# Kernel tuning notes

Measured on AMD Instinct MI355X. Metric: run time of the kernel, lower is better.

## Reference

```python
import jax, jax.numpy as jnp
import numpy as np

LMBD = 0.1      # cfg['MODEL']['LAMBDA'][0]
MU = 0.1        # ISTA/FISTA step size (cfg['MODEL']['MU'])
N_STEPS = 4     # cfg['MODEL']['NUM_LAYERS']
FISTA = True    # cfg['MODEL']['ISFISTA']


def _conv(x, W, s, p):
    # torch F.conv2d, NCHW / OIHW
    return jax.lax.conv_general_dilated(x, W, (s, s), [(p, p), (p, p)],
        dimension_numbers=('NCHW', 'OIHW', 'NCHW'))


def _conv_t(z, W, s, p):
    # torch F.conv_transpose2d(z, W, stride=s, padding=p): output (H-1)*s + k - 2p
    k = W.shape[-1]
    Wt = jnp.transpose(jnp.flip(W, (-2, -1)), (1, 0, 2, 3))
    pad = k - 1 - p
    return jax.lax.conv_general_dilated(z, Wt, (1, 1), [(pad, pad), (pad, pad)],
        lhs_dilation=(s, s), dimension_numbers=('NCHW', 'OIHW', 'NCHW'))


def _wnorm(W):
    # per-atom unit-norm dictionary (w_norm=True)
    return W / (jnp.sqrt(jnp.sum(W * W, axis=(1, 2, 3), keepdims=True)) + 1e-12)


def _dict_block(x, W, s, p):
    # unrolled FISTA sparse coding: min_z 0.5||x - W^T*z||^2 + lmbd||z||_1, z>=0
    thr = MU * LMBD
    shrink = lambda u: jax.nn.relu(u - thr)  # non-negative soft threshold
    z0 = shrink(MU * _conv(x, W, s, p))

    def body(carry, _):
        z, z_old, t = carry
        if FISTA:
            t_new = (1.0 + jnp.sqrt(1.0 + 4.0 * t * t)) * 0.5
            y = z + ((t - 1.0) / t_new) * (z - z_old)
        else:
            t_new, y = t, z
        r = x - _conv_t(y, W, s, p)                 # residual in image space
        z_new = shrink(y + MU * _conv(r, W, s, p))  # gradient step + shrinkage
        return (z_new, z, t_new), None

    (z, _, _), _ = jax.lax.scan(body, (z0, z0, jnp.float32(1.0)), None, length=N_STEPS - 1)
    return z


def _bn(x, eps=1e-5):
    # BatchNorm2d at init (gamma=1, beta=0), training-mode batch stats, biased var
    m = jnp.mean(x, axis=(0, 2, 3), keepdims=True)
    v = jnp.var(x, axis=(0, 2, 3), keepdims=True)
    return (x - m) * jax.lax.rsqrt(v + eps)


def _lrelu(x):
    return jnp.where(x >= 0, x, 0.2 * x)


def setup_inputs() -> dict:
    key = jax.random.key(0)
    ks = jax.random.split(key, 7)
    nc, ndf, nz = 3, 64, 128

    def kaiming(k, shape):
        fan_in = shape[1] * shape[2] * shape[3]
        bound = float(np.sqrt(6.0 / fan_in))
        return jax.random.uniform(k, shape, jnp.float32, -bound, bound)

    return {
        'x':  jax.random.normal(ks[0], (64, nc, 96, 96), jnp.float32),
        'W1': kaiming(ks[1], (ndf, nc, 4, 4)),
        'W2': kaiming(ks[2], (ndf * 2, ndf, 4, 4)),
        'W3': kaiming(ks[3], (ndf * 4, ndf * 2, 4, 4)),
        'W4': kaiming(ks[4], (ndf * 8, ndf * 4, 4, 4)),
        'W5': kaiming(ks[5], (ndf * 16, ndf * 8, 4, 4)),
        'W6': kaiming(ks[6], (nz, ndf * 16, 3, 3)),
    }


def reference(x, W1, W2, W3, W4, W5, W6):
    Ws = [_wnorm(w) for w in (W1, W2, W3, W4, W5, W6)]
    # encoder: 96 -> 48 -> 24 -> 12 -> 6 -> 3 -> 1
    o = _lrelu(_dict_block(x, Ws[0], 2, 1))
    for i in range(1, 5):
        o = _lrelu(_bn(_dict_block(o, Ws[i], 2, 1)))
    z = _dict_block(o, Ws[5], 1, 0).reshape(x.shape[0], -1)
    z = z / jnp.maximum(jnp.linalg.norm(z, axis=1, keepdims=True), 1e-12)  # F.normalize
    # decoder (DictConv2d.inverse chain, uses the normalized dictionaries)
    h = z.reshape(z.shape[0], -1, 1, 1)
    h = jax.nn.relu(_bn(_conv_t(h, Ws[5], 1, 0)))
    for i in (4, 3, 2, 1):
        h = jax.nn.relu(_bn(_conv_t(h, Ws[i], 2, 1)))
    x_hat = jnp.tanh(_conv_t(h, Ws[0], 2, 1))
    return z, x_hat
```

## Files before the change

kernel.cpp:

```cpp
#include <hip/hip_runtime.h>
#include <math.h>

#define BLK 256
static constexpr float MU_F  = 0.1f;
static constexpr float THR_F = 0.01f;

typedef __attribute__((ext_vector_type(8))) short bf16x8;
typedef __attribute__((ext_vector_type(4))) float f32x4;

__device__ inline unsigned short f2bf(float f) {
    unsigned u = __float_as_uint(f);
    unsigned r = (u + 0x7fffu + ((u >> 16) & 1u)) >> 16;
    return (unsigned short)r;
}
__device__ inline float bf2f(unsigned short h) {
    return __uint_as_float(((unsigned)h) << 16);
}

__device__ inline float blk_reduce(float v) {
    __shared__ float sh[BLK];
    int tid = threadIdx.x;
    sh[tid] = v;
    __syncthreads();
    #pragma unroll
    for (int s = BLK / 2; s > 0; s >>= 1) {
        if (tid < s) sh[tid] += sh[tid + s];
        __syncthreads();
    }
    float r = sh[0];
    __syncthreads();
    return r;
}

__global__ __launch_bounds__(BLK) void wnorm_pack(
    const float* __restrict__ W, float* __restrict__ Wkc,
    float* __restrict__ Wnout, int Mout, int asz)
{
    int o = blockIdx.x;
    const float* w = W + (size_t)o * asz;
    float s = 0.f;
    for (int i = threadIdx.x; i < asz; i += BLK) { float v = w[i]; s = fmaf(v, v, s); }
    float tot = blk_reduce(s);
    float inv = 1.0f / (sqrtf(tot) + 1e-12f);
    for (int i = threadIdx.x; i < asz; i += BLK) {
        float v = w[i] * inv;
        Wkc[(size_t)i * Mout + o] = v;
        if (Wnout) Wnout[(size_t)o * asz + i] = v;
    }
}

__global__ __launch_bounds__(BLK) void wnorm_pack_bf16(
    const float* __restrict__ W, short* __restrict__ Cpk, short* __restrict__ Tpk,
    int Cout, int Cin)
{
    int o = blockIdx.x;
    int asz = Cin * 16;
    const float* w = W + (size_t)o * asz;
    float s = 0.f;
    for (int i = threadIdx.x; i < asz; i += BLK) { float v = w[i]; s = fmaf(v, v, s); }
    float tot = blk_reduce(s);
    float inv = 1.0f / (sqrtf(tot) + 1e-12f);
    size_t cTot = (size_t)Cout * asz;
    size_t parStride = (size_t)Cout * 4 * Cin;
    size_t tTot = 4 * parStride;
    for (int i = threadIdx.x; i < asz; i += BLK) {
        float v = w[i] * inv;
        unsigned short hb = f2bf(v);
        unsigned short lb = f2bf(v - bf2f(hb));
        size_t cidx = ((size_t)(i >> 3)) * (Cout * 8) + o * 8 + (i & 7);
        Cpk[cidx] = (short)hb;
        Cpk[cTot + cidx] = (short)lb;
        int c = i >> 4, tap = i & 15, kh = tap >> 2, kw = tap & 3;
        int par = (1 - (kh & 1)) * 2 + (1 - (kw & 1));
        int tt = ((kh >> 1) << 1) | (kw >> 1);
        int q = o * 4 + tt;
        size_t tidx = (size_t)par * parStride + ((size_t)(q >> 3)) * (Cin * 8) + c * 8 + (q & 7);
        Tpk[tidx] = (short)hb;
        Tpk[tTot + tidx] = (short)lb;
    }
}

__device__ inline void xcd_remap(int& bx, int& by, int& bz) {
    int nx = gridDim.x, ny = gridDim.y;
    int nwg = nx * ny * gridDim.z;
    int orig = blockIdx.x + nx * (blockIdx.y + ny * blockIdx.z);
    int q8 = nwg >> 3, r8 = nwg & 7, xcd = orig & 7, sidx = orig >> 3;
    int w = (xcd < r8 ? xcd * (q8 + 1) : r8 * (q8 + 1) + (xcd - r8) * q8) + sidx;
    bx = w % nx; int t = w / nx; by = t % ny; bz = t / ny;
}

__global__ __launch_bounds__(BLK) void conv_gemm_bf16(
    const short* __restrict__ Wpk, const float* __restrict__ x,
    const float* __restrict__ yin, float* __restrict__ out,
    int M, int Cx, int Hx, int Wx, int Hout, int Wout,
    int kchunk, int emode)
{
    __shared__ __align__(16) short Wh[4][64][8];
    __shared__ __align__(16) short Wo_[4][64][8];
    __shared__ __align__(16) short Xh[4][64][8];
    __shared__ __align__(16) short Xo[4][64][8];
    int bx, by, bz; xcd_remap(bx, by, bz);
    int tid = threadIdx.x, lane = tid & 63, wid = tid >> 6;
    int HW = Hout * Wout, HWx = Hx * Wx;
    int pbase = bx * 64, m0 = by * 64, kb = bz * kchunk;
    size_t loOff = (size_t)Cx * 16 * M;

    int spl = tid & 63, skb = tid >> 6;
    int sp = pbase + spl;
    int sn = sp / HW; int srr = sp - sn * HW;
    int sho = srr / Wout, swo = srr - sho * Wout;
    const float* xs = x + (size_t)sn * Cx * HWx;
    int h0 = sho * 2 - 1, w0 = swo * 2 - 1;

    f32x4 acc[4] = {};
    for (int k0 = kb; k0 < kb + kchunk; k0 += 32) {
        size_t so = ((size_t)((k0 >> 3) + skb)) * (M * 8) + (size_t)m0 * 8 + spl * 8;
        *(float4*)(&Wh[skb][spl][0])  = *(const float4*)(Wpk + so);
        *(float4*)(&Wo_[skb][spl][0]) = *(const float4*)(Wpk + loOff + so);
        {
            int kbase = k0 + skb * 8;
            int ci = kbase >> 4;
            int t16 = kbase & 15;
            const float* xc = xs + (size_t)ci * HWx;
            union { short s[8]; float4 f; } uh, ul;
            #pragma unroll
            for (int jj = 0; jj < 8; ++jj) {
                int tap = t16 + jj;
                int kh = tap >> 2, kw = tap & 3;
                int h = h0 + kh, w = w0 + kw;
                float g = ((unsigned)h < (unsigned)Hx && (unsigned)w < (unsigned)Wx)
                        ? xc[h * Wx + w] : 0.f;
                unsigned short hb = f2bf(g);
                uh.s[jj] = (short)hb;
                ul.s[jj] = (short)f2bf(g - bf2f(hb));
            }
            *(float4*)(&Xh[skb][spl][0]) = uh.f;
            *(float4*)(&Xo[skb][spl][0]) = ul.f;
        }
        __syncthreads();
        bf16x8 ah = *(const bf16x8*)(&Wh[lane >> 4][wid * 16 + (lane & 15)][0]);
        bf16x8 al = *(const bf16x8*)(&Wo_[lane >> 4][wid * 16 + (lane & 15)][0]);
        #pragma unroll
        for (int nf = 0; nf < 4; ++nf) {
            bf16x8 bh = *(const bf16x8*)(&Xh[lane >> 4][nf * 16 + (lane & 15)][0]);
            bf16x8 bl = *(const bf16x8*)(&Xo[lane >> 4][nf * 16 + (lane & 15)][0]);
            acc[nf] = __builtin_amdgcn_mfma_f32_16x16x32_bf16(al, bh, acc[nf], 0, 0, 0);
            acc[nf] = __builtin_amdgcn_mfma_f32_16x16x32_bf16(ah, bl, acc[nf], 0, 0, 0);
            acc[nf] = __builtin_amdgcn_mfma_f32_16x16x32_bf16(ah, bh, acc[nf], 0, 0, 0);
        }
        __syncthreads();
    }
    int colp = lane & 15, rquad = lane >> 4;
    #pragma unroll
    for (int nf = 0; nf < 4; ++nf) {
        int p = pbase + nf * 16 + colp;
        int n = p / HW; int rr = p - n * HW;
        int ho = rr / Wout, wo = rr - ho * Wout;
        #pragma unroll
        for (int r = 0; r < 4; ++r) {
            int m = m0 + wid * 16 + rquad * 4 + r;
            size_t idx = (((size_t)n * M + m) * Hout + ho) * Wout + wo;
            float v = acc[nf][r];
            if (emode == 0)      out[idx] = fmaxf(MU_F * v - THR_F, 0.f);
            else if (emode == 1) out[idx] = fmaxf(yin[idx] + MU_F * v - THR_F, 0.f);
            else                 atomicAdd(&out[idx], v);
        }
    }
}

__global__ __launch_bounds__(BLK) void convt_gemm_bf16(
    const short* __restrict__ Wpk, const float* __restrict__ z,
    const float* __restrict__ aux, float* __restrict__ out,
    int M, int Cz, int Hz, int Wz, int Ho, int Wo, int emode, int SK)
{
    __shared__ __align__(16) short Wh[4][64][8];
    __shared__ __align__(16) short Wo_[4][64][8];
    __shared__ __align__(16) short Xh[4][64][8];
    __shared__ __align__(16) short Xo[4][64][8];
    int bx, by, bz; xcd_remap(bx, by, bz);
    int tid = threadIdx.x, lane = tid & 63, wid = tid >> 6;
    int par = bz / SK, chunk = bz - par * SK;
    int hbit = par >> 1, wbit = par & 1;
    int czs = Cz / SK;
    int qb = chunk * czs * 4;
    size_t parS = (size_t)Cz * 4 * M;
    const short* Wp = Wpk + (size_t)par * parS;
    size_t loOff = 4 * parS;
    int Hc = Ho >> 1, Wc = Wo >> 1, HWc = Hc * Wc;
    int pbase = bx * 64, m0 = by * 64;

    int spl = tid & 63, skb = tid >> 6;
    int sp = pbase + spl;
    int sn = sp / HWc; int srr = sp - sn * HWc;
    int shc = srr / Wc, swc = srr - shc * Wc;
    const float* zs = z + (size_t)sn * Cz * Hz * Wz;

    f32x4 acc[4] = {};
    for (int q0 = qb; q0 < qb + czs * 4; q0 += 32) {
        size_t so = ((size_t)((q0 >> 3) + skb)) * (M * 8) + (size_t)m0 * 8 + spl * 8;
        *(float4*)(&Wh[skb][spl][0])  = *(const float4*)(Wp + so);
        *(float4*)(&Wo_[skb][spl][0]) = *(const float4*)(Wp + loOff + so);
        {
            int qq = q0 + skb * 8;
            union { short s[8]; float4 f; } uh, ul;
            #pragma unroll
            for (int jj = 0; jj < 8; ++jj) {
                int q = qq + jj;
                int cz = q >> 2, tt = q & 3, ti = tt >> 1, tj = tt & 1;
                int hn = shc + hbit - ti, wn = swc + wbit - tj;
                float g = ((unsigned)hn < (unsigned)Hz && (unsigned)wn < (unsigned)Wz)
                        ? zs[((size_t)cz * Hz + hn) * Wz + wn] : 0.f;
                unsigned short hb = f2bf(g);
                uh.s[jj] = (short)hb;
                ul.s[jj] = (short)f2bf(g - bf2f(hb));
            }
            *(float4*)(&Xh[skb][spl][0]) = uh.f;
            *(float4*)(&Xo[skb][spl][0]) = ul.f;
        }
        __syncthreads();
        bf16x8 ah = *(const bf16x8*)(&Wh[lane >> 4][wid * 16 + (lane & 15)][0]);
        bf16x8 al = *(const bf16x8*)(&Wo_[lane >> 4][wid * 16 + (lane & 15)][0]);
        #pragma unroll
        for (int nf = 0; nf < 4; ++nf) {
            bf16x8 bh = *(const bf16x8*)(&Xh[lane >> 4][nf * 16 + (lane & 15)][0]);
            bf16x8 bl = *(const bf16x8*)(&Xo[lane >> 4][nf * 16 + (lane & 15)][0]);
            acc[nf] = __builtin_amdgcn_mfma_f32_16x16x32_bf16(al, bh, acc[nf], 0, 0, 0);
            acc[nf] = __builtin_amdgcn_mfma_f32_16x16x32_bf16(ah, bl, acc[nf], 0, 0, 0);
            acc[nf] = __builtin_amdgcn_mfma_f32_16x16x32_bf16(ah, bh, acc[nf], 0, 0, 0);
        }
        __syncthreads();
    }
    int colp = lane & 15, rquad = lane >> 4;
    #pragma unroll
    for (int nf = 0; nf < 4; ++nf) {
        int p = pbase + nf * 16 + colp;
        int n = p / HWc; int rr = p - n * HWc;
        int hc = rr / Wc, wc = rr - hc * Wc;
        int ho = 2 * hc + hbit, wo = 2 * wc + wbit;
        #pragma unroll
        for (int r = 0; r < 4; ++r) {
            int m = m0 + wid * 16 + rquad * 4 + r;
            size_t idx = (((size_t)n * M + m) * Ho + ho) * Wo + wo;
            float v = acc[nf][r];
            if (emode == 0)      out[idx] = aux[idx] - v;
            else if (emode == 1) out[idx] = v;
            else                 atomicAdd(&out[idx], v);
        }
    }
}

template <int KK, int Kk, int S, int P>
__global__ __launch_bounds__(BLK) void conv_gemm(
    const float* __restrict__ Wp, const float* __restrict__ x,
    const float* __restrict__ yin, float* __restrict__ out,
    int M, int Ktot, int Cx, int Hx, int Wx, int Hout, int Wout,
    int kchunk, int emode)
{
    __shared__ float Wt[16][64];
    __shared__ float Xt[16][64];
    int tid = threadIdx.x, tx = tid & 15, ty = tid >> 4;
    int HW = Hout * Wout, HWx = Hx * Wx;
    int pbase = blockIdx.x * 64 + tx * 4;
    int n_[4], ho_[4], wo_[4];
    const float* xb_[4];
    #pragma unroll
    for (int j = 0; j < 4; ++j) {
        int p = pbase + j; int n = p / HW; int r = p - n * HW;
        int ho = r / Wout; int wo = r - ho * Wout;
        n_[j] = n; ho_[j] = ho; wo_[j] = wo;
        xb_[j] = x + (size_t)n * Cx * HWx;
    }
    int m0 = blockIdx.y * 64;
    int kb = blockIdx.z * kchunk, ke = kb + kchunk;
    if (ke > Ktot) ke = Ktot;
    float acc[4][4] = {};
    for (int k0 = kb; k0 < ke; k0 += 16) {
        int kr = k0 + ty;
        *(float4*)&Wt[ty][tx * 4] = *(const float4*)&Wp[(size_t)kr * M + m0 + tx * 4];
        int ci = kr / KK; int t = kr - ci * KK; int kh = t / Kk; int kw = t - kh * Kk;
        int cio = ci * HWx;
        float g[4];
        #pragma unroll
        for (int j = 0; j < 4; ++j) {
            int h = ho_[j] * S - P + kh, w = wo_[j] * S - P + kw;
            g[j] = ((unsigned)h < (unsigned)Hx && (unsigned)w < (unsigned)Wx)
                 ? xb_[j][cio + h * Wx + w] : 0.f;
        }
        *(float4*)&Xt[ty][tx * 4] = make_float4(g[0], g[1], g[2], g[3]);
        __syncthreads();
        #pragma unroll
        for (int kk = 0; kk < 16; ++kk) {
            float4 a = *(float4*)&Wt[kk][ty * 4];
            float4 b = *(float4*)&Xt[kk][tx * 4];
            float aa[4] = {a.x, a.y, a.z, a.w};
            float bb[4] = {b.x, b.y, b.z, b.w};
            #pragma unroll
            for (int i = 0; i < 4; ++i)
                #pragma unroll
                for (int j = 0; j < 4; ++j)
                    acc[i][j] = fmaf(aa[i], bb[j], acc[i][j]);
        }
        __syncthreads();
    }
    #pragma unroll
    for (int i = 0; i < 4; ++i) {
        int m = m0 + ty * 4 + i;
        #pragma unroll
        for (int j = 0; j < 4; ++j) {
            size_t idx = (((size_t)n_[j] * M + m) * Hout + ho_[j]) * Wout + wo_[j];
            float v = acc[i][j];
            if (emode == 0)      out[idx] = fmaxf(MU_F * v - THR_F, 0.f);
            else if (emode == 1) out[idx] = fmaxf(yin[idx] + MU_F * v - THR_F, 0.f);
            else                 atomicAdd(&out[idx], v);
        }
    }
}

__global__ __launch_bounds__(BLK) void outer_gemm(
    const float* __restrict__ Wp, const float* __restrict__ zin,
    const float* __restrict__ aux, float* __restrict__ out,
    int M, int Kz, int emode)
{
    __shared__ float Wt[16][64];
    __shared__ float Xt[16][64];
    int tid = threadIdx.x, tx = tid & 15, ty = tid >> 4;
    int m0 = blockIdx.y * 64;
    float acc[4][4] = {};
    for (int k0 = 0; k0 < Kz; k0 += 16) {
        int kr = k0 + ty;
        *(float4*)&Wt[ty][tx * 4] = *(const float4*)&Wp[(size_t)kr * M + m0 + tx * 4];
        float g[4];
        #pragma unroll
        for (int j = 0; j < 4; ++j) g[j] = zin[(size_t)(tx * 4 + j) * Kz + kr];
        *(float4*)&Xt[ty][tx * 4] = make_float4(g[0], g[1], g[2], g[3]);
        __syncthreads();
        #pragma unroll
        for (int kk = 0; kk < 16; ++kk) {
            float4 a = *(float4*)&Wt[kk][ty * 4];
            float4 b = *(float4*)&Xt[kk][tx * 4];
            float aa[4] = {a.x, a.y, a.z, a.w};
            float bb[4] = {b.x, b.y, b.z, b.w};
            #pragma unroll
            for (int i = 0; i < 4; ++i)
                #pragma unroll
                for (int j = 0; j < 4; ++j)
                    acc[i][j] = fmaf(aa[i], bb[j], acc[i][j]);
        }
        __syncthreads();
    }
    #pragma unroll
    for (int i = 0; i < 4; ++i) {
        int m = m0 + ty * 4 + i;
        #pragma unroll
        for (int j = 0; j < 4; ++j) {
            int n = tx * 4 + j;
            size_t idx = (size_t)n * M + m;
            float v = acc[i][j];
            out[idx] = (emode == 0) ? (aux[idx] - v) : v;
        }
    }
}

__global__ __launch_bounds__(BLK) void convt_m3(
    const float* __restrict__ Wkc0, const float* __restrict__ z,
    const float* __restrict__ aux, float* __restrict__ out,
    int Cz, int Hz, int Wz, int Ho, int Wo, int emode)
{
    __shared__ float Wl[64 * 4 * 3];
    int tid = threadIdx.x;
    int hbit = blockIdx.z >> 1, wbit = blockIdx.z & 1;
    int khp = 1 - hbit, kwp = 1 - wbit;
    int Ktot = Cz * 4;
    for (int kidx = tid; kidx < Ktot; kidx += BLK) {
        int cz = kidx >> 2, t = kidx & 3, ti = t >> 1, tj = t & 1;
        int tap = (khp + 2 * ti) * 4 + (kwp + 2 * tj);
        Wl[kidx * 3 + 0] = Wkc0[(0 * 16 + tap) * 64 + cz];
        Wl[kidx * 3 + 1] = Wkc0[(1 * 16 + tap) * 64 + cz];
        Wl[kidx * 3 + 2] = Wkc0[(2 * 16 + tap) * 64 + cz];
    }
    __syncthreads();
    int Hc = Ho >> 1, Wc = Wo >> 1, HWc = Hc * Wc;
    int p = blockIdx.x * BLK + tid;
    int n = p / HWc, r = p - n * HWc, hc = r / Wc, wc = r - (r / Wc) * Wc;
    const float* zb = z + (size_t)n * Cz * Hz * Wz;
    int offs[4]; bool val[4];
    #pragma unroll
    for (int t = 0; t < 4; ++t) {
        int ti = t >> 1, tj = t & 1;
        int hn = hc + hbit - ti, wn = wc + wbit - tj;
        val[t] = ((unsigned)hn < (unsigned)Hz) && ((unsigned)wn < (unsigned)Wz);
        offs[t] = hn * Wz + wn;
    }
    float a0 = 0.f, a1 = 0.f, a2 = 0.f;
    int HWz = Hz * Wz;
    for (int cz = 0; cz < Cz; ++cz) {
        const float* base = zb + cz * HWz;
        #pragma unroll
        for (int t = 0; t < 4; ++t) {
            float g = val[t] ? base[offs[t]] : 0.f;
            int wi = (cz * 4 + t) * 3;
            a0 = fmaf(g, Wl[wi + 0], a0);
            a1 = fmaf(g, Wl[wi + 1], a1);
            a2 = fmaf(g, Wl[wi + 2], a2);
        }
    }
    int ho = 2 * hc + hbit, wo = 2 * wc + wbit;
    #pragma unroll
    for (int u = 0; u < 3; ++u) {
        float v = (u == 0) ? a0 : (u == 1) ? a1 : a2;
        size_t idx = (((size_t)n * 3 + u) * Ho + ho) * Wo + wo;
        out[idx] = (emode == 0) ? (aux[idx] - v) : tanhf(v);
    }
}

__global__ __launch_bounds__(BLK) void shrink_epi(
    const float* __restrict__ p, const float* __restrict__ y,
    float* __restrict__ o, int n, int mode)
{
    int i = blockIdx.x * BLK + threadIdx.x;
    if (i >= n) return;
    float v = MU_F * p[i] - THR_F;
    if (mode == 1) v += y[i];
    o[i] = fmaxf(v, 0.f);
}

__global__ __launch_bounds__(BLK) void res_epi(
    const float* __restrict__ aux, const float* __restrict__ acc,
    float* __restrict__ o, int n)
{
    int i = blockIdx.x * BLK + threadIdx.x;
    if (i >= n) return;
    o[i] = aux[i] - acc[i];
}

__global__ __launch_bounds__(BLK) void y_update_kernel(
    const float* __restrict__ z, const float* __restrict__ zo,
    float* __restrict__ y, int total, float c)
{
    int i = blockIdx.x * BLK + threadIdx.x;
    if (i >= total) return;
    float zv = z[i];
    y[i] = fmaf(c, zv - zo[i], zv);
}

__global__ __launch_bounds__(BLK) void bn_stats_kernel(
    const float* __restrict__ x, float* __restrict__ mean, float* __restrict__ rstd,
    int N, int C, int HW)
{
    int c = blockIdx.x;
    int cnt = N * HW;
    float s = 0.f, s2 = 0.f;
    for (int i = threadIdx.x; i < cnt; i += BLK) {
        int n = i / HW, hw = i - n * HW;
        float v = x[((size_t)n * C + c) * HW + hw];
        s += v; s2 = fmaf(v, v, s2);
    }
    float ts  = blk_reduce(s);
    float ts2 = blk_reduce(s2);
    if (threadIdx.x == 0) {
        float m = ts / cnt;
        float var = ts2 / cnt - m * m;
        mean[c] = m;
        rstd[c] = rsqrtf(var + 1e-5f);
    }
}

__global__ __launch_bounds__(BLK) void bn_act_kernel(
    const float* __restrict__ x, const float* __restrict__ mean,
    const float* __restrict__ rstd, float* __restrict__ out,
    int total, int C, int HW, int use_bn, int act)
{
    int i = blockIdx.x * BLK + threadIdx.x;
    if (i >= total) return;
    float v = x[i];
    if (use_bn) { int c = (i / HW) % C; v = (v - mean[c]) * rstd[c]; }
    out[i] = (act == 0) ? ((v >= 0.f) ? v : 0.2f * v) : fmaxf(v, 0.f);
}

__global__ __launch_bounds__(128) void rownorm_kernel(
    const float* __restrict__ z, float* __restrict__ out, float* __restrict__ zvec)
{
    __shared__ float sh[128];
    int r = blockIdx.x, tid = threadIdx.x;
    float v = z[r * 128 + tid];
    sh[tid] = v * v;
    __syncthreads();
    #pragma unroll
    for (int s = 64; s > 0; s >>= 1) {
        if (tid < s) sh[tid] += sh[tid + s];
        __syncthreads();
    }
    float nrm = fmaxf(sqrtf(sh[0]), 1e-12f);
    float o = v / nrm;
    out[r * 128 + tid] = o;
    zvec[r * 128 + tid] = o;
}

static inline int gdiv(int a, int b) { return (a + b - 1) / b; }

extern "C" void kernel_launch(void* const* d_in, const int* in_sizes, int n_in,
                              void* d_out, int out_size, void* d_ws, size_t ws_size,
                              hipStream_t stream)
{
    const float* x = (const float*)d_in[0];
    const float* W[6];
    for (int i = 0; i < 6; ++i) W[i] = (const float*)d_in[1 + i];
    float* ws  = (float*)d_ws;
    float* out = (float*)d_out;

    const int Cin[6]  = {3, 64, 128, 256, 512, 1024};
    const int Cout[6] = {64, 128, 256, 512, 1024, 128};
    const int Hin[6]  = {96, 48, 24, 12, 6, 3};
    const int Hout[6] = {48, 24, 12, 6, 3, 1};
    const int N = 64;
    const int SKc[6] = {1, 1, 2, 4, 8, 1};
    const int SKt[6] = {1, 1, 1, 2, 4, 1};

    size_t off = 0;
    float* Wkc0 = ws + off; off += 3072;
    float* Wkc5 = ws + off; off += 1179648;
    float* Wn5  = ws + off; off += 1179648;
    const size_t csz[5] = {0, 131072, 524288, 2097152, 8388608};
    short* Cpk[5]; short* Tpk[5];
    {
        short* sbase = (short*)(ws + off);
        size_t soff = 0;
        for (int L = 1; L < 5; ++L) { Cpk[L] = sbase + soff; soff += 2 * csz[L]; }
        for (int L = 1; L < 5; ++L) { Tpk[L] = sbase + soff; soff += 2 * csz[L]; }
        off += soff / 2;
    }
    const size_t POOL = 30081024;
    float* pool = ws + off; off += POOL;
    float* xb   = ws + off; off += 9437184;
    float* mean = ws + off; off += 1024;
    float* rstd = ws + off; off += 1024;
    float* zvec = ws + off; off += 8192;
    float* pbuf = ws + off; off += 2359296;

    wnorm_pack<<<64, BLK, 0, stream>>>(W[0], Wkc0, nullptr, 64, 48);
    for (int L = 1; L < 5; ++L)
        wnorm_pack_bf16<<<Cout[L], BLK, 0, stream>>>(W[L], Cpk[L], Tpk[L], Cout[L], Cin[L]);
    wnorm_pack<<<128, BLK, 0, stream>>>(W[5], Wkc5, Wn5, 128, 9216);

    double td = 1.0; float cc[3];
    for (int i = 0; i < 3; ++i) {
        double tn = (1.0 + sqrt(1.0 + 4.0 * td * td)) * 0.5;
        cc[i] = (float)((td - 1.0) / tn);
        td = tn;
    }

    const float* in = x;
    for (int L = 0; L < 6; ++L) {
        int zTot = N * Cout[L] * Hout[L] * Hout[L];
        int xTot = N * Cin[L] * Hin[L] * Hin[L];
        int npix = N * Hout[L] * Hout[L];
        dim3 ge(gdiv(zTot, BLK));
        dim3 gr(gdiv(xTot, BLK));

        float* zA = pool;
        float* zB = pool + (size_t)zTot;
        float* yb = pool + (size_t)2 * zTot;
        float* rb = pool + (size_t)3 * zTot;

        auto launch_conv = [&](const float* src, const float* y, float* dst, int mode) {
            if (L == 5) {
                hipMemsetAsync(pbuf, 0, (size_t)zTot * 4, stream);
                conv_gemm<9, 3, 1, 0><<<dim3(1, 2, 72), BLK, 0, stream>>>(Wkc5, src,
                    nullptr, pbuf, 128, 9216, 1024, 3, 3, 1, 1, 128, 2);
                shrink_epi<<<gdiv(zTot, BLK), BLK, 0, stream>>>(pbuf, y, dst, zTot, mode);
            } else if (L == 0) {
                conv_gemm<16, 4, 2, 1><<<dim3(npix / 64, 1), BLK, 0, stream>>>(
                    Wkc0, src, y, dst, 64, 48, 3, 96, 96, 48, 48, 48, mode);
            } else if (SKc[L] == 1) {
                conv_gemm_bf16<<<dim3(npix / 64, Cout[L] / 64), BLK, 0, stream>>>(
                    Cpk[L], src, y, dst, Cout[L], Cin[L], Hin[L], Hin[L],
                    Hout[L], Hout[L], Cin[L] * 16, mode);
            } else {
                int sk = SKc[L];
                hipMemsetAsync(pbuf, 0, (size_t)zTot * 4, stream);
                conv_gemm_bf16<<<dim3(npix / 64, Cout[L] / 64, sk), BLK, 0, stream>>>(
                    Cpk[L], src, nullptr, pbuf, Cout[L], Cin[L], Hin[L], Hin[L],
                    Hout[L], Hout[L], Cin[L] * 16 / sk, 2);
                shrink_epi<<<gdiv(zTot, BLK), BLK, 0, stream>>>(pbuf, y, dst, zTot, mode);
            }
        };

        launch_conv(in, nullptr, zA, 0);

        float* z = zA; float* zo = zB;
        for (int it = 0; it < 3; ++it) {
            const float* zold = (it == 0) ? z : zo;
            y_update_kernel<<<ge, BLK, 0, stream>>>(z, zold, yb, zTot, cc[it]);
            if (L == 0) {
                convt_m3<<<dim3(N * 48 * 48 / BLK, 1, 4), BLK, 0, stream>>>(
                    Wkc0, yb, in, rb, 64, 48, 48, 96, 96, 0);
            } else if (L < 5) {
                int xpixc = N * (Hin[L] / 2) * (Hin[L] / 2);
                int sk = SKt[L];
                if (sk == 1) {
                    convt_gemm_bf16<<<dim3(xpixc / 64, Cin[L] / 64, 4), BLK, 0, stream>>>(
                        Tpk[L], yb, in, rb, Cin[L], Cout[L], Hout[L], Hout[L],
                        Hin[L], Hin[L], 0, 1);
                } else {
                    hipMemsetAsync(rb, 0, (size_t)xTot * 4, stream);
                    convt_gemm_bf16<<<dim3(xpixc / 64, Cin[L] / 64, 4 * sk), BLK, 0, stream>>>(
                        Tpk[L], yb, nullptr, rb, Cin[L], Cout[L], Hout[L], Hout[L],
                        Hin[L], Hin[L], 2, sk);
                    res_epi<<<gr, BLK, 0, stream>>>(in, rb, rb, xTot);
                }
            } else {
                outer_gemm<<<dim3(1, 144), BLK, 0, stream>>>(Wn5, yb, in, rb, 9216, 128, 0);
            }
            launch_conv(rb, yb, zo, 1);
            float* tmp = z; z = zo; zo = tmp;
        }

        int HW = Hout[L] * Hout[L];
        if (L == 0) {
            bn_act_kernel<<<ge, BLK, 0, stream>>>(z, nullptr, nullptr, xb, zTot, Cout[L], HW, 0, 0);
            in = xb;
        } else if (L < 5) {
            bn_stats_kernel<<<Cout[L], BLK, 0, stream>>>(z, mean, rstd, N, Cout[L], HW);
            bn_act_kernel<<<ge, BLK, 0, stream>>>(z, mean, rstd, xb, zTot, Cout[L], HW, 1, 0);
            in = xb;
        } else {
            rownorm_kernel<<<64, 128, 0, stream>>>(z, out, zvec);
        }
    }

    float* zA = pool;
    float* zB = pool + 9437184;
    {
        int oT = N * 1024 * 9;
        outer_gemm<<<dim3(1, 144), BLK, 0, stream>>>(Wn5, zvec, nullptr, zA, 9216, 128, 1);
        bn_stats_kernel<<<1024, BLK, 0, stream>>>(zA, mean, rstd, N, 1024, 9);
        bn_act_kernel<<<gdiv(oT, BLK), BLK, 0, stream>>>(zA, mean, rstd, zB, oT, 1024, 9, 1, 1);
    }
    float* cur = zB;
    for (int i = 4; i >= 1; --i) {
        int oT = N * Cin[i] * Hin[i] * Hin[i];
        int xpixc = N * (Hin[i] / 2) * (Hin[i] / 2);
        int sk = SKt[i];
        if (sk == 1) {
            convt_gemm_bf16<<<dim3(xpixc / 64, Cin[i] / 64, 4), BLK, 0, stream>>>(
                Tpk[i], cur, nullptr, zA, Cin[i], Cout[i], Hout[i], Hout[i],
                Hin[i], Hin[i], 1, 1);
        } else {
            hipMemsetAsync(zA, 0, (size_t)oT * 4, stream);
            convt_gemm_bf16<<<dim3(xpixc / 64, Cin[i] / 64, 4 * sk), BLK, 0, stream>>>(
                Tpk[i], cur, nullptr, zA, Cin[i], Cout[i], Hout[i], Hout[i],
                Hin[i], Hin[i], 2, sk);
        }
        bn_stats_kernel<<<Cin[i], BLK, 0, stream>>>(zA, mean, rstd, N, Cin[i], Hin[i] * Hin[i]);
        bn_act_kernel<<<gdiv(oT, BLK), BLK, 0, stream>>>(zA, mean, rstd, zB, oT,
            Cin[i], Hin[i] * Hin[i], 1, 1);
        cur = zB;
    }
    convt_m3<<<dim3(N * 48 * 48 / BLK, 1, 4), BLK, 0, stream>>>(
        Wkc0, cur, nullptr, out + 8192, 64, 48, 48, 96, 96, 2);
}
```

Baseline: 4.319 ms.

## Vectorize elementwise kernels, split BN stats across blocks, skip first y update

The elementwise kernels (shrink, residual, y update, BN apply) now load and store float4 instead of scalars. BN statistics are split over several blocks per channel, which accumulate partial sums with atomics before a separate finalize kernel, so low-channel layers get more parallelism. The first FISTA y update is skipped because its coefficient is zero, and z is used directly. The changes cut memory transactions and launches but add a memset and a finalize launch per BN, and they assume element counts divisible by four.

Result: faster. 3.985 ms (-7.7%).

```diff
diff --git a/kernel.cpp b/kernel.cpp
--- a/kernel.cpp
+++ b/kernel.cpp
@@ -413,44 +413,61 @@
     }
 }
 
-__global__ __launch_bounds__(BLK) void shrink_epi(
+__global__ __launch_bounds__(BLK) void shrink_epi_v4(
     const float* __restrict__ p, const float* __restrict__ y,
-    float* __restrict__ o, int n, int mode)
+    float* __restrict__ o, int n4, int mode)
 {
     int i = blockIdx.x * BLK + threadIdx.x;
-    if (i >= n) return;
-    float v = MU_F * p[i] - THR_F;
-    if (mode == 1) v += y[i];
-    o[i] = fmaxf(v, 0.f);
-}
-
-__global__ __launch_bounds__(BLK) void res_epi(
+    if (i >= n4) return;
+    float4 pv = ((const float4*)p)[i];
+    float4 r;
+    if (mode == 1) {
+        float4 yv = ((const float4*)y)[i];
+        r.x = fmaxf(yv.x + MU_F * pv.x - THR_F, 0.f);
+        r.y = fmaxf(yv.y + MU_F * pv.y - THR_F, 0.f);
+        r.z = fmaxf(yv.z + MU_F * pv.z - THR_F, 0.f);
+        r.w = fmaxf(yv.w + MU_F * pv.w - THR_F, 0.f);
+    } else {
+        r.x = fmaxf(MU_F * pv.x - THR_F, 0.f);
+        r.y = fmaxf(MU_F * pv.y - THR_F, 0.f);
+        r.z = fmaxf(MU_F * pv.z - THR_F, 0.f);
+        r.w = fmaxf(MU_F * pv.w - THR_F, 0.f);
+    }
+    ((float4*)o)[i] = r;
+}
+
+__global__ __launch_bounds__(BLK) void res_epi_v4(
     const float* __restrict__ aux, const float* __restrict__ acc,
-    float* __restrict__ o, int n)
+    float* __restrict__ o, int n4)
 {
     int i = blockIdx.x * BLK + threadIdx.x;
-    if (i >= n) return;
-    o[i] = aux[i] - acc[i];
-}
-
-__global__ __launch_bounds__(BLK) void y_update_kernel(
+    if (i >= n4) return;
+    float4 a = ((const float4*)aux)[i];
+    float4 b = ((const float4*)acc)[i];
+    ((float4*)o)[i] = make_float4(a.x - b.x, a.y - b.y, a.z - b.z, a.w - b.w);
+}
+
+__global__ __launch_bounds__(BLK) void y_update_v4(
     const float* __restrict__ z, const float* __restrict__ zo,
-    float* __restrict__ y, int total, float c)
+    float* __restrict__ y, int n4, float c)
 {
     int i = blockIdx.x * BLK + threadIdx.x;
-    if (i >= total) return;
-    float zv = z[i];
-    y[i] = fmaf(c, zv - zo[i], zv);
-}
-
-__global__ __launch_bounds__(BLK) void bn_stats_kernel(
-    const float* __restrict__ x, float* __restrict__ mean, float* __restrict__ rstd,
-    int N, int C, int HW)
-{
-    int c = blockIdx.x;
+    if (i >= n4) return;
+    float4 zv = ((const float4*)z)[i];
+    float4 ov = ((const float4*)zo)[i];
+    ((float4*)y)[i] = make_float4(
+        fmaf(c, zv.x - ov.x, zv.x), fmaf(c, zv.y - ov.y, zv.y),
+        fmaf(c, zv.z - ov.z, zv.z), fmaf(c, zv.w - ov.w, zv.w));
+}
+
+__global__ __launch_bounds__(BLK) void bn_stats_part(
+    const float* __restrict__ x, float* __restrict__ stats,
+    int N, int C, int HW, int nblk)
+{
+    int c = blockIdx.x, b = blockIdx.y;
     int cnt = N * HW;
     float s = 0.f, s2 = 0.f;
-    for (int i = threadIdx.x; i < cnt; i += BLK) {
+    for (int i = b * BLK + threadIdx.x; i < cnt; i += nblk * BLK) {
         int n = i / HW, hw = i - n * HW;
         float v = x[((size_t)n * C + c) * HW + hw];
         s += v; s2 = fmaf(v, v, s2);
@@ -458,23 +475,39 @@
     float ts  = blk_reduce(s);
     float ts2 = blk_reduce(s2);
     if (threadIdx.x == 0) {
-        float m = ts / cnt;
-        float var = ts2 / cnt - m * m;
-        mean[c] = m;
-        rstd[c] = rsqrtf(var + 1e-5f);
-    }
-}
-
-__global__ __launch_bounds__(BLK) void bn_act_kernel(
+        atomicAdd(&stats[c], ts);
+        atomicAdd(&stats[C + c], ts2);
+    }
+}
+__global__ __launch_bounds__(BLK) void bn_finalize(
+    const float* __restrict__ stats, float* __restrict__ mean,
+    float* __restrict__ rstd, int C, int cnt)
+{
+    int c = blockIdx.x * BLK + threadIdx.x;
+    if (c >= C) return;
+    float m = stats[c] / cnt;
+    float var = stats[C + c] / cnt - m * m;
+    mean[c] = m;
+    rstd[c] = rsqrtf(var + 1e-5f);
+}
+
+__global__ __launch_bounds__(BLK) void bn_act_v4(
     const float* __restrict__ x, const float* __restrict__ mean,
     const float* __restrict__ rstd, float* __restrict__ out,
-    int total, int C, int HW, int use_bn, int act)
+    int n4, int C, int HW, int use_bn, int act)
 {
     int i = blockIdx.x * BLK + threadIdx.x;
-    if (i >= total) return;
-    float v = x[i];
-    if (use_bn) { int c = (i / HW) % C; v = (v - mean[c]) * rstd[c]; }
-    out[i] = (act == 0) ? ((v >= 0.f) ? v : 0.2f * v) : fmaxf(v, 0.f);
+    if (i >= n4) return;
+    float4 v = ((const float4*)x)[i];
+    float e[4] = {v.x, v.y, v.z, v.w};
+    int base = i * 4;
+    #pragma unroll
+    for (int j = 0; j < 4; ++j) {
+        float t = e[j];
+        if (use_bn) { int c = ((base + j) / HW) % C; t = (t - mean[c]) * rstd[c]; }
+        e[j] = (act == 0) ? ((t >= 0.f) ? t : 0.2f * t) : fmaxf(t, 0.f);
+    }
+    ((float4*)out)[i] = make_float4(e[0], e[1], e[2], e[3]);
 }
 
 __global__ __launch_bounds__(128) void rownorm_kernel(
@@ -534,6 +567,7 @@
     float* xb   = ws + off; off += 9437184;
     float* mean = ws + off; off += 1024;
     float* rstd = ws + off; off += 1024;
+    float* stats= ws + off; off += 2048;
     float* zvec = ws + off; off += 8192;
     float* pbuf = ws + off; off += 2359296;
 
@@ -549,13 +583,22 @@
         td = tn;
     }
 
+    auto run_bn_stats = [&](const float* src, int C, int HW) {
+        int cnt = N * HW;
+        int nblk = 2048 / C; if (nblk < 1) nblk = 1;
+        int maxb = gdiv(cnt, BLK); if (nblk > maxb) nblk = maxb;
+        hipMemsetAsync(stats, 0, 2 * C * sizeof(float), stream);
+        bn_stats_part<<<dim3(C, nblk), BLK, 0, stream>>>(src, stats, N, C, HW, nblk);
+        bn_finalize<<<gdiv(C, BLK), BLK, 0, stream>>>(stats, mean, rstd, C, cnt);
+    };
+
     const float* in = x;
     for (int L = 0; L < 6; ++L) {
         int zTot = N * Cout[L] * Hout[L] * Hout[L];
         int xTot = N * Cin[L] * Hin[L] * Hin[L];
         int npix = N * Hout[L] * Hout[L];
-        dim3 ge(gdiv(zTot, BLK));
-        dim3 gr(gdiv(xTot, BLK));
+        dim3 ge4(gdiv(zTot / 4, BLK));
+        dim3 gr4(gdiv(xTot / 4, BLK));
 
         float* zA = pool;
         float* zB = pool + (size_t)zTot;
@@ -567,7 +610,7 @@
                 hipMemsetAsync(pbuf, 0, (size_t)zTot * 4, stream);
                 conv_gemm<9, 3, 1, 0><<<dim3(1, 2, 72), BLK, 0, stream>>>(Wkc5, src,
                     nullptr, pbuf, 128, 9216, 1024, 3, 3, 1, 1, 128, 2);
-                shrink_epi<<<gdiv(zTot, BLK), BLK, 0, stream>>>(pbuf, y, dst, zTot, mode);
+                shrink_epi_v4<<<gdiv(zTot / 4, BLK), BLK, 0, stream>>>(pbuf, y, dst, zTot / 4, mode);
             } else if (L == 0) {
                 conv_gemm<16, 4, 2, 1><<<dim3(npix / 64, 1), BLK, 0, stream>>>(
                     Wkc0, src, y, dst, 64, 48, 3, 96, 96, 48, 48, 48, mode);
@@ -581,7 +624,7 @@
                 conv_gemm_bf16<<<dim3(npix / 64, Cout[L] / 64, sk), BLK, 0, stream>>>(
                     Cpk[L], src, nullptr, pbuf, Cout[L], Cin[L], Hin[L], Hin[L],
                     Hout[L], Hout[L], Cin[L] * 16 / sk, 2);
-                shrink_epi<<<gdiv(zTot, BLK), BLK, 0, stream>>>(pbuf, y, dst, zTot, mode);
+                shrink_epi_v4<<<gdiv(zTot / 4, BLK), BLK, 0, stream>>>(pbuf, y, dst, zTot / 4, mode);
             }
         };
 
@@ -589,39 +632,44 @@
 
         float* z = zA; float* zo = zB;
         for (int it = 0; it < 3; ++it) {
-            const float* zold = (it == 0) ? z : zo;
-            y_update_kernel<<<ge, BLK, 0, stream>>>(z, zold, yb, zTot, cc[it]);
+            const float* ybp;
+            if (it == 0) {
+                ybp = z;
+            } else {
+                y_update_v4<<<ge4, BLK, 0, stream>>>(z, zo, yb, zTot / 4, cc[it]);
+                ybp = yb;
+            }
             if (L == 0) {
                 convt_m3<<<dim3(N * 48 * 48 / BLK, 1, 4), BLK, 0, stream>>>(
-                    Wkc0, yb, in, rb, 64, 48, 48, 96, 96, 0);
+                    Wkc0, ybp, in, rb, 64, 48, 48, 96, 96, 0);
             } else if (L < 5) {
                 int xpixc = N * (Hin[L] / 2) * (Hin[L] / 2);
                 int sk = SKt[L];
                 if (sk == 1) {
                     convt_gemm_bf16<<<dim3(xpixc / 64, Cin[L] / 64, 4), BLK, 0, stream>>>(
-                        Tpk[L], yb, in, rb, Cin[L], Cout[L], Hout[L], Hout[L],
+                        Tpk[L], ybp, in, rb, Cin[L], Cout[L], Hout[L], Hout[L],
                         Hin[L], Hin[L], 0, 1);
                 } else {
                     hipMemsetAsync(rb, 0, (size_t)xTot * 4, stream);
                     convt_gemm_bf16<<<dim3(xpixc / 64, Cin[L] / 64, 4 * sk), BLK, 0, stream>>>(
-                        Tpk[L], yb, nullptr, rb, Cin[L], Cout[L], Hout[L], Hout[L],
+                        Tpk[L], ybp, nullptr, rb, Cin[L], Cout[L], Hout[L], Hout[L],
                         Hin[L], Hin[L], 2, sk);
-                    res_epi<<<gr, BLK, 0, stream>>>(in, rb, rb, xTot);
+                    res_epi_v4<<<gr4, BLK, 0, stream>>>(in, rb, rb, xTot / 4);
                 }
             } else {
-                outer_gemm<<<dim3(1, 144), BLK, 0, stream>>>(Wn5, yb, in, rb, 9216, 128, 0);
+                outer_gemm<<<dim3(1, 144), BLK, 0, stream>>>(Wn5, ybp, in, rb, 9216, 128, 0);
             }
-            launch_conv(rb, yb, zo, 1);
+            launch_conv(rb, ybp, zo, 1);
             float* tmp = z; z = zo; zo = tmp;
         }
 
         int HW = Hout[L] * Hout[L];
         if (L == 0) {
-            bn_act_kernel<<<ge, BLK, 0, stream>>>(z, nullptr, nullptr, xb, zTot, Cout[L], HW, 0, 0);
+            bn_act_v4<<<ge4, BLK, 0, stream>>>(z, nullptr, nullptr, xb, zTot / 4, Cout[L], HW, 0, 0);
             in = xb;
         } else if (L < 5) {
-            bn_stats_kernel<<<Cout[L], BLK, 0, stream>>>(z, mean, rstd, N, Cout[L], HW);
-            bn_act_kernel<<<ge, BLK, 0, stream>>>(z, mean, rstd, xb, zTot, Cout[L], HW, 1, 0);
+            run_bn_stats(z, Cout[L], HW);
+            bn_act_v4<<<ge4, BLK, 0, stream>>>(z, mean, rstd, xb, zTot / 4, Cout[L], HW, 1, 0);
             in = xb;
         } else {
             rownorm_kernel<<<64, 128, 0, stream>>>(z, out, zvec);
@@ -633,8 +681,8 @@
     {
         int oT = N * 1024 * 9;
         outer_gemm<<<dim3(1, 144), BLK, 0, stream>>>(Wn5, zvec, nullptr, zA, 9216, 128, 1);
-        bn_stats_kernel<<<1024, BLK, 0, stream>>>(zA, mean, rstd, N, 1024, 9);
-        bn_act_kernel<<<gdiv(oT, BLK), BLK, 0, stream>>>(zA, mean, rstd, zB, oT, 1024, 9, 1, 1);
+        run_bn_stats(zA, 1024, 9);
+        bn_act_v4<<<gdiv(oT / 4, BLK), BLK, 0, stream>>>(zA, mean, rstd, zB, oT / 4, 1024, 9, 1, 1);
     }
     float* cur = zB;
     for (int i = 4; i >= 1; --i) {
@@ -651,8 +699,8 @@
                 Tpk[i], cur, nullptr, zA, Cin[i], Cout[i], Hout[i], Hout[i],
                 Hin[i], Hin[i], 2, sk);
         }
-        bn_stats_kernel<<<Cin[i], BLK, 0, stream>>>(zA, mean, rstd, N, Cin[i], Hin[i] * Hin[i]);
-        bn_act_kernel<<<gdiv(oT, BLK), BLK, 0, stream>>>(zA, mean, rstd, zB, oT,
+        run_bn_stats(zA, Cin[i], Hin[i] * Hin[i]);
+        bn_act_v4<<<gdiv(oT / 4, BLK), BLK, 0, stream>>>(zA, mean, rstd, zB, oT / 4,
             Cin[i], Hin[i] * Hin[i], 1, 1);
         cur = zB;
     }
```
